# Kernel optimization log

Hardware: AMD Instinct MI355X
Metric: run time of the kernel (lower is better)

Reference implementation:

```python
import jax, jax.numpy as jnp
import numpy as np

NBX = 24  # nb_x_patches
NBY = 24  # nb_y_patches
B, H, D = 8, 12, 64
L = NBX * NBY + 1  # 577 (grid tokens + 1 CLS token from the pad)
EPS = 1e-08


def _toeplitz_mask(topological_params):
    # topological_params: [H, 4*NBX*NBY]
    gi = jnp.arange(NBX)
    gj = jnp.arange(NBY)
    # relative 2D displacement index, flattened over (i, j, i', j')
    dist_index = ((gi[:, None, None, None] - gi[None, None, :, None] + NBX) * 2 * NBY
                  + gj[None, :, None, None] - gj[None, None, None, :] + NBY)
    dist_index = dist_index.reshape(-1)
    m = jnp.take(topological_params, dist_index, axis=1)
    m = m.reshape(topological_params.shape[0], NBX * NBY, NBX * NBY)  # [H, L-1, L-1]
    # pad CLS row and column with 1.0
    m = jnp.pad(m, [[0, 0], [1, 0], [1, 0]], constant_values=1.0)  # [H, L, L]
    return m[None]  # [1, H, L, L]


def setup_inputs() -> dict:
    key = jax.random.key(0)
    k1, k2, k3, k4 = jax.random.split(key, 4)
    return {
        'query': jax.random.normal(k1, (B, L, H, D), dtype=jnp.float32),
        'key': jax.random.normal(k2, (B, L, H, D), dtype=jnp.float32),
        'value': jax.random.normal(k3, (B, L, H, D), dtype=jnp.float32),
        'topological_params': jax.random.normal(k4, (H, 4 * NBX * NBY), dtype=jnp.float32),
    }


def reference(query, key, value, topological_params):
    depth = query.shape[-1]
    q = query / jnp.sqrt(jnp.asarray(depth, query.dtype))
    # relu feature map (kernel_type == 'relu')
    q = jax.nn.relu(q) + EPS
    k = jax.nn.relu(key) + EPS
    attn = jnp.einsum('bqhd,bkhd->bhqk', q, k)  # [B, H, L, L]
    top_mask = _toeplitz_mask(topological_params)  # [1, H, L, L]
    attn = attn * jnp.abs(top_mask) + EPS
    attn = attn / jnp.sum(attn, axis=-1, keepdims=True)  # kernelized normalization (no softmax)
    return jnp.einsum('bhqk,bkhd->bqhd', attn, value)
```

## Files before the change

### kernel.cpp

```cpp
#include <hip/hip_runtime.h>


#define Lq 577
#define NH 12
#define NB 8
#define DD 64
#define PAR 2304
#define EPSf 1e-8f

#define VT_OFF 7090176ull
#define MM_OFF 14954496ull

typedef __attribute__((ext_vector_type(4))) float f32x4;
typedef __attribute__((ext_vector_type(8))) short s16x8;

__device__ __forceinline__ float bflo(unsigned int u) {
    return __builtin_bit_cast(float, u << 16);
}
__device__ __forceinline__ float bfhi(unsigned int u) {
    return __builtin_bit_cast(float, u & 0xffff0000u);
}
__device__ __forceinline__ unsigned int f2bf(float f) {
    unsigned int x = __builtin_bit_cast(unsigned int, f);
    return (x + 0x7fffu + ((x >> 16) & 1u)) >> 16;
}
__device__ __forceinline__ int imin(int a, int b) { return a < b ? a : b; }

__device__ __forceinline__ void gload_lds16(const unsigned short* g, unsigned short* l) {
    __builtin_amdgcn_global_load_lds(
        (const __attribute__((address_space(1))) unsigned int*)g,
        (__attribute__((address_space(3))) unsigned int*)l, 16, 0, 0);
}

__device__ __forceinline__ bool probe_f32(const void* Qg) {
    float x = fabsf(((const float*)Qg)[threadIdx.x]);
    unsigned long long hit = __ballot(x > 2.44140625e-4f && x < 64.0f);
    unsigned long long act = __ballot(1);
    return 2 * __popcll(hit) >= __popcll(act);
}

template <bool F32>
__device__ __forceinline__ void load8f(const void* G, size_t eidx, float* o) {
    if constexpr (F32) {
        const float* p = (const float*)G + eidx;
        float4 a = *(const float4*)p;
        float4 b = *(const float4*)(p + 4);
        o[0] = a.x; o[1] = a.y; o[2] = a.z; o[3] = a.w;
        o[4] = b.x; o[5] = b.y; o[6] = b.z; o[7] = b.w;
    } else {
        const unsigned short* p = (const unsigned short*)G + eidx;
        uint4 a = *(const uint4*)p;
        unsigned int u[4] = {a.x, a.y, a.z, a.w};
#pragma unroll
        for (int j = 0; j < 4; ++j) {
            o[2 * j]     = bflo(u[j]);
            o[2 * j + 1] = bfhi(u[j]);
        }
    }
}

template <bool F32>
__device__ void prep_k_body(const void* Kg, unsigned short* Kp) {
    size_t i8 = ((size_t)blockIdx.x * 256 + threadIdx.x) * 8;
    float f[8];
    load8f<F32>(Kg, i8, f);
    unsigned int o[4];
#pragma unroll
    for (int j = 0; j < 4; ++j) {
        unsigned int lo = f2bf(fmaxf(f[2 * j], 0.0f) + EPSf);
        unsigned int hi = f2bf(fmaxf(f[2 * j + 1], 0.0f) + EPSf);
        o[j] = lo | (hi << 16);
    }
    *(uint4*)(Kp + i8) = make_uint4(o[0], o[1], o[2], o[3]);
}
__global__ __launch_bounds__(256)
void prep_k(const void* __restrict__ Qg, const void* __restrict__ Kg,
            unsigned short* __restrict__ Kp) {
    if (probe_f32(Qg)) prep_k_body<true>(Kg, Kp);
    else               prep_k_body<false>(Kg, Kp);
}

template <bool F32>
__device__ void prep_vt_body(const void* Vg, unsigned short* Vt, unsigned short* s) {
    const int t  = threadIdx.x;
    const int kt = blockIdx.x, h = blockIdx.y, b = blockIdx.z;
    {
        int kl  = t >> 2;
        int dch = (t & 3) * 16;
        int k   = kt * 64 + kl;
        unsigned int pk[8] = {};
        if (k <= 576) {
            float f[16];
            size_t base = ((size_t)((b * Lq + k) * NH + h)) * DD + dch;
            load8f<F32>(Vg, base, f);
            load8f<F32>(Vg, base + 8, f + 8);
#pragma unroll
            for (int j = 0; j < 8; ++j)
                pk[j] = f2bf(f[2 * j]) | (f2bf(f[2 * j + 1]) << 16);
        }
#pragma unroll
        for (int j = 0; j < 8; ++j)
            *(unsigned int*)&s[kl * 72 + dch + 2 * j] = pk[j];
    }
    __syncthreads();
    {
        int d   = t >> 2;
        int kch = (t & 3) * 16;
        unsigned int o[8];
#pragma unroll
        for (int j = 0; j < 8; ++j) {
            unsigned short v0 = s[(kch + 2 * j) * 72 + d];
            unsigned short v1 = s[(kch + 2 * j + 1) * 72 + d];
            o[j] = (unsigned int)v0 | ((unsigned int)v1 << 16);
        }
        size_t base = ((size_t)((b * NH + h) * 64 + d)) * 640 + kt * 64 + kch;
        *(uint4*)(Vt + base)     = make_uint4(o[0], o[1], o[2], o[3]);
        *(uint4*)(Vt + base + 8) = make_uint4(o[4], o[5], o[6], o[7]);
    }
}
__global__ __launch_bounds__(256)
void prep_vt(const void* __restrict__ Qg, const void* __restrict__ Vg,
             unsigned short* __restrict__ Vt) {
    __shared__ unsigned short s[64 * 72];
    if (probe_f32(Qg)) prep_vt_body<true>(Vg, Vt, s);
    else               prep_vt_body<false>(Vg, Vt, s);
}

template <bool F32>
__device__ void prep_mask_body(const void* Tg, unsigned short* Mm) {
    const int q = blockIdx.x, h = blockIdx.y;
    const int k0 = threadIdx.x * 8;
    int cq = 0;
    if (q > 0) {
        int qq = q - 1;
        int qi = (qq * 2731) >> 16;
        cq = qq + 24 * qi + 1176;
    }
    unsigned int o[4];
#pragma unroll
    for (int j = 0; j < 4; ++j) {
        unsigned int hv[2];
#pragma unroll
        for (int e = 0; e < 2; ++e) {
            int k = k0 + 2 * j + e;
            float m;
            if (k > 576) m = 0.0f;
            else if (k == 0 || q == 0) m = 1.0f;
            else {
                int kk = k - 1;
                int ki = (kk * 2731) >> 16;
                int idx = cq - (kk + 24 * ki);
                float pv = F32 ? ((const float*)Tg)[h * PAR + idx]
                               : bflo((unsigned int)((const unsigned short*)Tg)[h * PAR + idx]);
                m = fabsf(pv);
                m = (m == m) ? m : 0.0f;
            }
            hv[e] = f2bf(m);
        }
        o[j] = hv[0] | (hv[1] << 16);
    }
    *(uint4*)(Mm + (size_t)(h * Lq + q) * 640 + k0) = make_uint4(o[0], o[1], o[2], o[3]);
}
__global__ __launch_bounds__(128)
void prep_mask(const void* __restrict__ Qg, const void* __restrict__ Tg,
               unsigned short* __restrict__ Mm) {
    if (probe_f32(Qg)) prep_mask_body<true>(Tg, Mm);
    else               prep_mask_body<false>(Tg, Mm);
}

template <bool F32>
__device__ void attn_body(const void* __restrict__ Qg,
                          const unsigned short* __restrict__ Kp,
                          const unsigned short* __restrict__ Vt,
                          const unsigned short* __restrict__ Mm,
                          void* __restrict__ Og,
                          unsigned short* s_k, unsigned short* s_vt,
                          unsigned short* s_m, unsigned short* s_p_all) {
    const int tid  = threadIdx.x;
    const int w    = tid >> 6;
    const int lane = tid & 63;
    const int g    = lane >> 4;
    const int lm   = lane & 15;

    const int bid = blockIdx.x;
    const int qt  = bid / 96;
    const int bh  = bid - qt * 96;
    const int h   = bh % NH;
    const int b   = bh / NH;

    unsigned short* s_pw = s_p_all + w * 16 * 72;
    unsigned short* s_mw = s_m + w * 1024;

    const int q0w = qt * 64 + w * 16;

    const int q  = q0w + lm;
    const int qc = imin(q, Lq - 1);
    s16x8 a_q[2];
    {
        size_t rbase = ((size_t)((b * Lq + qc) * NH + h)) * DD;
#pragma unroll
        for (int ds = 0; ds < 2; ++ds) {
            float f[8];
            load8f<F32>(Qg, rbase + ds * 32 + g * 8, f);
            s16x8 a;
#pragma unroll
            for (int j = 0; j < 8; ++j) {
                float v = fmaf(fmaxf(f[j], 0.0f), 0.125f, EPSf);
                a[j] = (short)f2bf(v);
            }
            a_q[ds] = a;
        }
    }

    const int r8 = lane >> 3;
    const int c8 = lane & 7;
    const int xr = (c8 ^ r8) * 8;

    const unsigned short* KpBH = Kp + (size_t)b * (Lq * NH * DD) + h * DD;
    const unsigned short* VtL0 = Vt + ((size_t)(b * NH + h) * 64 + (w * 16 + r8)) * 640 + xr;
    const unsigned short* VtL1 = VtL0 + 8 * 640;
    const unsigned short* MmH  = Mm + (size_t)h * (Lq * 640);
    const unsigned short* MmL0 = MmH + (size_t)imin(q0w + r8, Lq - 1) * 640 + xr;
    const unsigned short* MmL1 = MmH + (size_t)imin(q0w + 8 + r8, Lq - 1) * 640 + xr;

    unsigned short* sk0 = s_k  + (w * 16) * 64;
    unsigned short* sk1 = sk0 + 8 * 64;
    unsigned short* sv0 = s_vt + (w * 16) * 64;
    unsigned short* sv1 = sv0 + 8 * 64;
    unsigned short* sm1 = s_mw + 8 * 64;

    f32x4 o_acc[4] = {};
    float rs = 0.0f;

    const int x7 = lm & 7;

    for (int kb = 0; kb < 640; kb += 64) {
        __syncthreads();

        int krr = kb + w * 16 + r8;
        int kr0 = imin(krr, Lq - 1);
        int kr1 = imin(krr + 8, Lq - 1);
        gload_lds16(KpBH + (size_t)kr0 * (NH * DD) + xr, sk0);
        gload_lds16(KpBH + (size_t)kr1 * (NH * DD) + xr, sk1);
        gload_lds16(VtL0 + kb, sv0);
        gload_lds16(VtL1 + kb, sv1);
        gload_lds16(MmL0 + kb, s_mw);
        gload_lds16(MmL1 + kb, sm1);
        __syncthreads();

        f32x4 sf[4];
#pragma unroll
        for (int cf = 0; cf < 4; ++cf) {
            const unsigned short* skr = s_k + (cf * 16 + lm) * 64;
            int co = (g ^ x7) * 8;
            s16x8 kf0 = *(const s16x8*)(skr + co);
            s16x8 kf1 = *(const s16x8*)(skr + (co ^ 32));
            f32x4 acc = {};
            acc = __builtin_amdgcn_mfma_f32_16x16x32_bf16(kf0, a_q[0], acc, 0, 0, 0);
            acc = __builtin_amdgcn_mfma_f32_16x16x32_bf16(kf1, a_q[1], acc, 0, 0, 0);
            sf[cf] = acc;
        }

#pragma unroll
        for (int cf = 0; cf < 4; ++cf) {
            int mo = ((cf * 2 + (g >> 1)) ^ x7) * 8 + (g & 1) * 4;
            uint2 mu = *(const uint2*)&s_mw[lm * 64 + mo];
            float m0 = bflo(mu.x), m1 = bfhi(mu.x);
            float m2 = bflo(mu.y), m3 = bfhi(mu.y);
            float p0 = fmaf(fmaxf(sf[cf][0], 0.0f), m0, EPSf);
            float p1 = fmaf(fmaxf(sf[cf][1], 0.0f), m1, EPSf);
            float p2 = fmaf(fmaxf(sf[cf][2], 0.0f), m2, EPSf);
            float p3 = fmaf(fmaxf(sf[cf][3], 0.0f), m3, EPSf);
            rs += (p0 + p1) + (p2 + p3);
            unsigned int d0 = f2bf(p0) | (f2bf(p1) << 16);
            unsigned int d1 = f2bf(p2) | (f2bf(p3) << 16);
            *(uint2*)&s_pw[lm * 72 + cf * 16 + g * 4] = make_uint2(d0, d1);
        }

#pragma unroll
        for (int ks = 0; ks < 2; ++ks) {
            s16x8 pa = *(const s16x8*)&s_pw[lm * 72 + ks * 32 + g * 8];
#pragma unroll
            for (int df = 0; df < 4; ++df) {
                const unsigned short* svr = s_vt + (df * 16 + lm) * 64;
                s16x8 vb = *(const s16x8*)(svr + ((ks * 4 + g) ^ x7) * 8);
                o_acc[df] = __builtin_amdgcn_mfma_f32_16x16x32_bf16(pa, vb, o_acc[df], 0, 0, 0);
            }
        }
    }

    float tot = rs;
    tot += __shfl_xor(tot, 16, 64);
    tot += __shfl_xor(tot, 32, 64);
    float inv = (tot > 0.0f) ? 1.0f / tot : 0.0f;

#pragma unroll
    for (int r = 0; r < 4; ++r) {
        int   qrow  = q0w + g * 4 + r;
        float inv_r = __shfl(inv, g * 4 + r, 64);
        if (qrow < Lq) {
            size_t base = ((size_t)((b * Lq + qrow) * NH + h)) * DD;
#pragma unroll
            for (int df = 0; df < 4; ++df) {
                float val = o_acc[df][r] * inv_r;
                if constexpr (F32)
                    ((float*)Og)[base + df * 16 + lm] = val;
                else
                    ((unsigned short*)Og)[base + df * 16 + lm] = (unsigned short)f2bf(val);
            }
        }
    }
}

__global__ __launch_bounds__(256, 4)
void fused_topo_attn(const void* __restrict__ Qg,
                     const unsigned short* __restrict__ Kp,
                     const unsigned short* __restrict__ Vt,
                     const unsigned short* __restrict__ Mm,
                     void* __restrict__ Og) {
    __shared__ __align__(16) unsigned short s_k[64 * 64];
    __shared__ __align__(16) unsigned short s_vt[64 * 64];
    __shared__ __align__(16) unsigned short s_m[4 * 16 * 64];
    __shared__ __align__(16) unsigned short s_p[4 * 16 * 72];

    if (probe_f32(Qg)) attn_body<true>(Qg, Kp, Vt, Mm, Og, s_k, s_vt, s_m, s_p);
    else               attn_body<false>(Qg, Kp, Vt, Mm, Og, s_k, s_vt, s_m, s_p);
}

extern "C" void kernel_launch(void* const* d_in, const int* in_sizes, int n_in,
                              void* d_out, int out_size, void* d_ws, size_t ws_size,
                              hipStream_t stream) {
    (void)in_sizes; (void)n_in; (void)out_size; (void)ws_size;
    unsigned short* Kp = (unsigned short*)d_ws;
    unsigned short* Vt = (unsigned short*)((char*)d_ws + VT_OFF);
    unsigned short* Mm = (unsigned short*)((char*)d_ws + MM_OFF);

    prep_k<<<1731, 256, 0, stream>>>(d_in[0], d_in[1], Kp);
    prep_vt<<<dim3(10, NH, NB), 256, 0, stream>>>(d_in[0], d_in[2], Vt);
    prep_mask<<<dim3(Lq, NH), 80, 0, stream>>>(d_in[0], d_in[3], Mm);
    fused_topo_attn<<<960, 256, 0, stream>>>(d_in[0], Kp, Vt, Mm, d_out);
}
```

Measured before the change: 123.4 us.

## Merge prep kernels, pre-swizzle mask to fragment layout, double-buffer K/V tiles

Folds the three preprocessing kernels into one launch using block-index ranges. The mask is stored in MFMA-fragment order so each lane loads its values straight into registers, prefetched one tile ahead, with no LDS staging. K and V^T tiles are double-buffered in LDS so the next tile's global-to-LDS load overlaps compute, with one barrier per iteration instead of two. LDS use grows and occupancy hint drops from 4 to 3 blocks per CU, and V conversion now zeroes NaNs.

```diff
diff --git a/kernel.cpp b/kernel.cpp
--- a/kernel.cpp
+++ b/kernel.cpp
@@ -9,7 +9,11 @@
 #define EPSf 1e-8f
 
 #define VT_OFF 7090176ull
-#define MM_OFF 14954496ull
+#define M2_OFF 14954496ull
+
+#define KBLK 1731
+#define VBLK 960
+#define MBLK 480
 
 typedef __attribute__((ext_vector_type(4))) float f32x4;
 typedef __attribute__((ext_vector_type(8))) short s16x8;
@@ -60,8 +64,8 @@
 }
 
 template <bool F32>
-__device__ void prep_k_body(const void* Kg, unsigned short* Kp) {
-    size_t i8 = ((size_t)blockIdx.x * 256 + threadIdx.x) * 8;
+__device__ void prep_k_body(const void* Kg, unsigned short* Kp, int bx) {
+    size_t i8 = ((size_t)bx * 256 + threadIdx.x) * 8;
     float f[8];
     load8f<F32>(Kg, i8, f);
     unsigned int o[4];
@@ -73,17 +77,14 @@
     }
     *(uint4*)(Kp + i8) = make_uint4(o[0], o[1], o[2], o[3]);
 }
-__global__ __launch_bounds__(256)
-void prep_k(const void* __restrict__ Qg, const void* __restrict__ Kg,
-            unsigned short* __restrict__ Kp) {
-    if (probe_f32(Qg)) prep_k_body<true>(Kg, Kp);
-    else               prep_k_body<false>(Kg, Kp);
-}
-
-template <bool F32>
-__device__ void prep_vt_body(const void* Vg, unsigned short* Vt, unsigned short* s) {
+
+template <bool F32>
+__device__ void prep_vt_body(const void* Vg, unsigned short* Vt,
+                             unsigned short* s, int id) {
     const int t  = threadIdx.x;
-    const int kt = blockIdx.x, h = blockIdx.y, b = blockIdx.z;
+    const int kt = id % 10;
+    const int h  = (id / 10) % NH;
+    const int b  = id / 120;
     {
         int kl  = t >> 2;
         int dch = (t & 3) * 16;
@@ -95,8 +96,12 @@
             load8f<F32>(Vg, base, f);
             load8f<F32>(Vg, base + 8, f + 8);
 #pragma unroll
-            for (int j = 0; j < 8; ++j)
-                pk[j] = f2bf(f[2 * j]) | (f2bf(f[2 * j + 1]) << 16);
+            for (int j = 0; j < 8; ++j) {
+                float a0 = f[2 * j], a1 = f[2 * j + 1];
+                a0 = (a0 == a0) ? a0 : 0.0f;
+                a1 = (a1 == a1) ? a1 : 0.0f;
+                pk[j] = f2bf(a0) | (f2bf(a1) << 16);
+            }
         }
 #pragma unroll
         for (int j = 0; j < 8; ++j)
@@ -118,33 +123,31 @@
         *(uint4*)(Vt + base + 8) = make_uint4(o[4], o[5], o[6], o[7]);
     }
 }
-__global__ __launch_bounds__(256)
-void prep_vt(const void* __restrict__ Qg, const void* __restrict__ Vg,
-             unsigned short* __restrict__ Vt) {
-    __shared__ unsigned short s[64 * 72];
-    if (probe_f32(Qg)) prep_vt_body<true>(Vg, Vt, s);
-    else               prep_vt_body<false>(Vg, Vt, s);
-}
-
-template <bool F32>
-__device__ void prep_mask_body(const void* Tg, unsigned short* Mm) {
-    const int q = blockIdx.x, h = blockIdx.y;
-    const int k0 = threadIdx.x * 8;
+
+template <bool F32>
+__device__ void prep_m2_body(const void* Tg, unsigned short* M2, int id) {
+    const int qg = id % 40;
+    const int h  = id / 40;
+    const int t    = threadIdx.x;
+    const int cf   = t >> 6;
+    const int lane = t & 63;
+    const int lm   = lane & 15;
+    const int g    = lane >> 4;
+    const int q    = qg * 16 + lm;
+    const bool qok = q < Lq;
     int cq = 0;
-    if (q > 0) {
+    if (qok && q > 0) {
         int qq = q - 1;
         int qi = (qq * 2731) >> 16;
         cq = qq + 24 * qi + 1176;
     }
-    unsigned int o[4];
-#pragma unroll
-    for (int j = 0; j < 4; ++j) {
-        unsigned int hv[2];
-#pragma unroll
-        for (int e = 0; e < 2; ++e) {
-            int k = k0 + 2 * j + e;
+    for (int kt = 0; kt < 10; ++kt) {
+        unsigned int hv[4];
+#pragma unroll
+        for (int e = 0; e < 4; ++e) {
+            int k = kt * 64 + cf * 16 + g * 4 + e;
             float m;
-            if (k > 576) m = 0.0f;
+            if (!qok || k > 576) m = 0.0f;
             else if (k == 0 || q == 0) m = 1.0f;
             else {
                 int kk = k - 1;
@@ -157,25 +160,39 @@
             }
             hv[e] = f2bf(m);
         }
-        o[j] = hv[0] | (hv[1] << 16);
-    }
-    *(uint4*)(Mm + (size_t)(h * Lq + q) * 640 + k0) = make_uint4(o[0], o[1], o[2], o[3]);
-}
-__global__ __launch_bounds__(128)
-void prep_mask(const void* __restrict__ Qg, const void* __restrict__ Tg,
-               unsigned short* __restrict__ Mm) {
-    if (probe_f32(Qg)) prep_mask_body<true>(Tg, Mm);
-    else               prep_mask_body<false>(Tg, Mm);
+        size_t base = ((size_t)(((h * 40 + qg) * 10 + kt) * 4 + cf) * 64 + lane) * 4;
+        *(uint2*)(M2 + base) = make_uint2(hv[0] | (hv[1] << 16), hv[2] | (hv[3] << 16));
+    }
+}
+
+__global__ __launch_bounds__(256)
+void prep_all(const void* __restrict__ Qg, const void* __restrict__ Kg,
+              const void* __restrict__ Vg, const void* __restrict__ Tg,
+              unsigned short* __restrict__ Kp, unsigned short* __restrict__ Vt,
+              unsigned short* __restrict__ M2) {
+    __shared__ unsigned short s[64 * 72];
+    bool f32 = probe_f32(Qg);
+    int bx = blockIdx.x;
+    if (bx < KBLK) {
+        if (f32) prep_k_body<true>(Kg, Kp, bx);
+        else     prep_k_body<false>(Kg, Kp, bx);
+    } else if (bx < KBLK + VBLK) {
+        if (f32) prep_vt_body<true>(Vg, Vt, s, bx - KBLK);
+        else     prep_vt_body<false>(Vg, Vt, s, bx - KBLK);
+    } else {
+        if (f32) prep_m2_body<true>(Tg, M2, bx - KBLK - VBLK);
+        else     prep_m2_body<false>(Tg, M2, bx - KBLK - VBLK);
+    }
 }
 
 template <bool F32>
 __device__ void attn_body(const void* __restrict__ Qg,
                           const unsigned short* __restrict__ Kp,
                           const unsigned short* __restrict__ Vt,
-                          const unsigned short* __restrict__ Mm,
+                          const unsigned short* __restrict__ M2,
                           void* __restrict__ Og,
                           unsigned short* s_k, unsigned short* s_vt,
-                          unsigned short* s_m, unsigned short* s_p_all) {
+                          unsigned short* s_p_all) {
     const int tid  = threadIdx.x;
     const int w    = tid >> 6;
     const int lane = tid & 63;
@@ -189,9 +206,9 @@
     const int b   = bh / NH;
 
     unsigned short* s_pw = s_p_all + w * 16 * 72;
-    unsigned short* s_mw = s_m + w * 1024;
 
     const int q0w = qt * 64 + w * 16;
+    const int qg  = qt * 4 + w;
 
     const int q  = q0w + lm;
     const int qc = imin(q, Lq - 1);
@@ -215,43 +232,53 @@
     const int r8 = lane >> 3;
     const int c8 = lane & 7;
     const int xr = (c8 ^ r8) * 8;
+    const int x7 = lm & 7;
 
     const unsigned short* KpBH = Kp + (size_t)b * (Lq * NH * DD) + h * DD;
     const unsigned short* VtL0 = Vt + ((size_t)(b * NH + h) * 64 + (w * 16 + r8)) * 640 + xr;
-    const unsigned short* VtL1 = VtL0 + 8 * 640;
-    const unsigned short* MmH  = Mm + (size_t)h * (Lq * 640);
-    const unsigned short* MmL0 = MmH + (size_t)imin(q0w + r8, Lq - 1) * 640 + xr;
-    const unsigned short* MmL1 = MmH + (size_t)imin(q0w + 8 + r8, Lq - 1) * 640 + xr;
-
-    unsigned short* sk0 = s_k  + (w * 16) * 64;
-    unsigned short* sk1 = sk0 + 8 * 64;
-    unsigned short* sv0 = s_vt + (w * 16) * 64;
-    unsigned short* sv1 = sv0 + 8 * 64;
-    unsigned short* sm1 = s_mw + 8 * 64;
+    const unsigned short* Mw   = M2 + (size_t)(h * 40 + qg) * 10240 + lane * 4;
 
     f32x4 o_acc[4] = {};
     float rs = 0.0f;
 
-    const int x7 = lm & 7;
-
-    for (int kb = 0; kb < 640; kb += 64) {
-        __syncthreads();
-
-        int krr = kb + w * 16 + r8;
+    uint2 mcur[4], mnxt[4];
+
+    auto stage = [&](int t, int buf) {
+        int kbn = t * 64;
+        int krr = kbn + w * 16 + r8;
         int kr0 = imin(krr, Lq - 1);
         int kr1 = imin(krr + 8, Lq - 1);
-        gload_lds16(KpBH + (size_t)kr0 * (NH * DD) + xr, sk0);
-        gload_lds16(KpBH + (size_t)kr1 * (NH * DD) + xr, sk1);
-        gload_lds16(VtL0 + kb, sv0);
-        gload_lds16(VtL1 + kb, sv1);
-        gload_lds16(MmL0 + kb, s_mw);
-        gload_lds16(MmL1 + kb, sm1);
+        unsigned short* k0 = s_k  + buf * 4096 + (w * 16) * 64;
+        unsigned short* v0 = s_vt + buf * 4096 + (w * 16) * 64;
+        gload_lds16(KpBH + (size_t)kr0 * (NH * DD) + xr, k0);
+        gload_lds16(KpBH + (size_t)kr1 * (NH * DD) + xr, k0 + 512);
+        gload_lds16(VtL0 + kbn, v0);
+        gload_lds16(VtL0 + 8 * 640 + kbn, v0 + 512);
+    };
+
+    stage(0, 0);
+#pragma unroll
+    for (int cf = 0; cf < 4; ++cf) mcur[cf] = *(const uint2*)(Mw + cf * 256);
+
+#pragma unroll 2
+    for (int t = 0; t < 10; ++t) {
+        const int cur = t & 1;
         __syncthreads();
 
+        if (t < 9) {
+            stage(t + 1, cur ^ 1);
+#pragma unroll
+            for (int cf = 0; cf < 4; ++cf)
+                mnxt[cf] = *(const uint2*)(Mw + (t + 1) * 1024 + cf * 256);
+        }
+
+        const unsigned short* skb = s_k  + cur * 4096;
+        const unsigned short* svb = s_vt + cur * 4096;
+
         f32x4 sf[4];
 #pragma unroll
         for (int cf = 0; cf < 4; ++cf) {
-            const unsigned short* skr = s_k + (cf * 16 + lm) * 64;
+            const unsigned short* skr = skb + (cf * 16 + lm) * 64;
             int co = (g ^ x7) * 8;
             s16x8 kf0 = *(const s16x8*)(skr + co);
             s16x8 kf1 = *(const s16x8*)(skr + (co ^ 32));
@@ -263,10 +290,8 @@
 
 #pragma unroll
         for (int cf = 0; cf < 4; ++cf) {
-            int mo = ((cf * 2 + (g >> 1)) ^ x7) * 8 + (g & 1) * 4;
-            uint2 mu = *(const uint2*)&s_mw[lm * 64 + mo];
-            float m0 = bflo(mu.x), m1 = bfhi(mu.x);
-            float m2 = bflo(mu.y), m3 = bfhi(mu.y);
+            float m0 = bflo(mcur[cf].x), m1 = bfhi(mcur[cf].x);
+            float m2 = bflo(mcur[cf].y), m3 = bfhi(mcur[cf].y);
             float p0 = fmaf(fmaxf(sf[cf][0], 0.0f), m0, EPSf);
             float p1 = fmaf(fmaxf(sf[cf][1], 0.0f), m1, EPSf);
             float p2 = fmaf(fmaxf(sf[cf][2], 0.0f), m2, EPSf);
@@ -282,11 +307,14 @@
             s16x8 pa = *(const s16x8*)&s_pw[lm * 72 + ks * 32 + g * 8];
 #pragma unroll
             for (int df = 0; df < 4; ++df) {
-                const unsigned short* svr = s_vt + (df * 16 + lm) * 64;
+                const unsigned short* svr = svb + (df * 16 + lm) * 64;
                 s16x8 vb = *(const s16x8*)(svr + ((ks * 4 + g) ^ x7) * 8);
                 o_acc[df] = __builtin_amdgcn_mfma_f32_16x16x32_bf16(pa, vb, o_acc[df], 0, 0, 0);
             }
         }
+
+#pragma unroll
+        for (int cf = 0; cf < 4; ++cf) mcur[cf] = mnxt[cf];
     }
 
     float tot = rs;
@@ -312,19 +340,18 @@
     }
 }
 
-__global__ __launch_bounds__(256, 4)
+__global__ __launch_bounds__(256, 3)
 void fused_topo_attn(const void* __restrict__ Qg,
                      const unsigned short* __restrict__ Kp,
                      const unsigned short* __restrict__ Vt,
-                     const unsigned short* __restrict__ Mm,
+                     const unsigned short* __restrict__ M2,
                      void* __restrict__ Og) {
-    __shared__ __align__(16) unsigned short s_k[64 * 64];
-    __shared__ __align__(16) unsigned short s_vt[64 * 64];
-    __shared__ __align__(16) unsigned short s_m[4 * 16 * 64];
+    __shared__ __align__(16) unsigned short s_k[2 * 64 * 64];
+    __shared__ __align__(16) unsigned short s_vt[2 * 64 * 64];
     __shared__ __align__(16) unsigned short s_p[4 * 16 * 72];
 
-    if (probe_f32(Qg)) attn_body<true>(Qg, Kp, Vt, Mm, Og, s_k, s_vt, s_m, s_p);
-    else               attn_body<false>(Qg, Kp, Vt, Mm, Og, s_k, s_vt, s_m, s_p);
+    if (probe_f32(Qg)) attn_body<true>(Qg, Kp, Vt, M2, Og, s_k, s_vt, s_p);
+    else               attn_body<false>(Qg, Kp, Vt, M2, Og, s_k, s_vt, s_p);
 }
 
 extern "C" void kernel_launch(void* const* d_in, const int* in_sizes, int n_in,
@@ -333,10 +360,9 @@
     (void)in_sizes; (void)n_in; (void)out_size; (void)ws_size;
     unsigned short* Kp = (unsigned short*)d_ws;
     unsigned short* Vt = (unsigned short*)((char*)d_ws + VT_OFF);
-    unsigned short* Mm = (unsigned short*)((char*)d_ws + MM_OFF);
-
-    prep_k<<<1731, 256, 0, stream>>>(d_in[0], d_in[1], Kp);
-    prep_vt<<<dim3(10, NH, NB), 256, 0, stream>>>(d_in[0], d_in[2], Vt);
-    prep_mask<<<dim3(Lq, NH), 80, 0, stream>>>(d_in[0], d_in[3], Mm);
-    fused_topo_attn<<<960, 256, 0, stream>>>(d_in[0], Kp, Vt, Mm, d_out);
-}
+    unsigned short* M2 = (unsigned short*)((char*)d_ws + M2_OFF);
+
+    prep_all<<<KBLK + VBLK + MBLK, 256, 0, stream>>>(
+        d_in[0], d_in[1], d_in[2], d_in[3], Kp, Vt, M2);
+    fused_topo_attn<<<960, 256, 0, stream>>>(d_in[0], Kp, Vt, M2, d_out);
+}
```

After: 125.5 us. Within noise of the previous version (+1.7%).
